# Optimization experiments

Measured on AMD Instinct MI355X. Metric: run time of the kernel, lower is better.

The kernel has to match this reference:

```python
import jax, jax.numpy as jnp
import numpy as np

NTOKENS = 50257
NHID = 1024
NPC = int(np.ceil(np.sqrt(NTOKENS)))            # 225 tokens per class
NCLASSES = int(np.ceil(NTOKENS / NPC))          # 224 classes
BATCH = 1024
INITRANGE = 0.1


def setup_inputs() -> dict:
    key = jax.random.key(0)
    k1, k2, k3, k4 = jax.random.split(key, 4)
    inputs = jax.random.normal(k1, (BATCH, NHID), dtype=jnp.float32)
    labels = jax.random.randint(k2, (BATCH,), 0, NTOKENS, dtype=jnp.int64)
    layer_top_W = jax.random.uniform(k3, (NHID, NCLASSES), minval=-INITRANGE, maxval=INITRANGE, dtype=jnp.float32)
    layer_top_b = jnp.zeros((NCLASSES,), dtype=jnp.float32)
    layer_bottom_W = jax.random.uniform(k4, (NCLASSES, NHID, NPC), minval=-INITRANGE, maxval=INITRANGE, dtype=jnp.float32)
    layer_bottom_b = jnp.zeros((NCLASSES, NPC), dtype=jnp.float32)
    return {
        "inputs": inputs,
        "labels": labels,
        "layer_top_W": layer_top_W,
        "layer_top_b": layer_top_b,
        "layer_bottom_W": layer_bottom_W,
        "layer_bottom_b": layer_bottom_b,
    }


def reference(inputs, labels, layer_top_W, layer_top_b, layer_bottom_W, layer_bottom_b):
    batch_size = inputs.shape[0]
    # decompose label into (class, within-class) position; old-torch `/` on Long == floor div
    pos_top = labels // NPC            # [B]
    pos_bottom = labels % NPC          # [B]

    # top-level class distribution: [B, nclasses]
    top_logits = inputs @ layer_top_W + layer_top_b
    top_probs = jax.nn.softmax(top_logits, axis=1)

    # gather per-sample class weight slices and do batched matvec:
    # layer_bottom_W[pos_top]: [B, nhid, npc]
    bottom_logits = jnp.einsum("bd,bdc->bc", inputs, layer_bottom_W[pos_top]) + layer_bottom_b[pos_top]
    bottom_probs = jax.nn.softmax(bottom_logits, axis=1)

    rows = jnp.arange(batch_size)
    target_probs = top_probs[rows, pos_top] * bottom_probs[rows, pos_bottom]  # [B]
    return target_probs
```

## Files before the change

kernel.cpp:

```cpp
#include <hip/hip_runtime.h>
#include <math.h>

#define NTOK 50257
#define NHID 1024
#define NPC  225
#define NCLS 224
#define BATCH 1024

#define WS_ORDER_OFS 16
#define WS_ITEMS_OFS 8192
#define WS_PTOP_OFS  16384
#define MAX_ITEMS    352

__global__ __launch_bounds__(256) void k0_group(const int* __restrict__ labels,
                                                int* __restrict__ ws)
{
    __shared__ int cnt[256];
    __shared__ int scan[256];
    __shared__ int iscan[256];
    __shared__ int cur[256];
    const int tid = threadIdx.x;

    cnt[tid] = 0;
    __syncthreads();
    for (int i = tid; i < BATCH; i += 256)
        atomicAdd(&cnt[labels[i] / NPC], 1);
    __syncthreads();

    const int myc = (tid < NCLS) ? cnt[tid] : 0;
    const int myi = (myc + 7) >> 3;
    scan[tid]  = myc;
    iscan[tid] = myi;
    __syncthreads();
    for (int off = 1; off < 256; off <<= 1) {
        int a = (tid >= off) ? scan[tid - off]  : 0;
        int b = (tid >= off) ? iscan[tid - off] : 0;
        __syncthreads();
        scan[tid]  += a;
        iscan[tid] += b;
        __syncthreads();
    }
    const int sbase = scan[tid]  - myc;
    const int ibase = iscan[tid] - myi;
    if (tid == 255) ws[0] = iscan[255];
    cur[tid] = sbase;

    int4* items = (int4*)((char*)ws + WS_ITEMS_OFS);
    if (tid < NCLS) {
        for (int t = 0; t < myi; ++t)
            items[ibase + t] = make_int4(tid, sbase + 8 * t, min(8, myc - 8 * t), 0);
    }
    __syncthreads();

    int* order = ws + WS_ORDER_OFS;
    for (int i = tid; i < BATCH; i += 256) {
        int c = labels[i] / NPC;
        int p = atomicAdd(&cur[c], 1);
        order[p] = i;
    }
}

__global__ __launch_bounds__(256) void k1_top(const float* __restrict__ X,
                                              const int* __restrict__ labels,
                                              const float* __restrict__ Wt,
                                              const float* __restrict__ bt,
                                              float* __restrict__ ptop)
{
    __shared__ __align__(16) float smem[12288];
    const int tid  = threadIdx.x;
    const int wave = tid >> 6;
    const int lane = tid & 63;
    const int sbase = blockIdx.x * 8;

    for (int idx = tid; idx < 8 * NHID; idx += 256) {
        int j = idx >> 10, dd = idx & 1023;
        smem[dd * 12 + j] = X[(sbase + j) * NHID + dd];
    }
    __syncthreads();

    float acc[8][4];
#pragma unroll
    for (int j = 0; j < 8; ++j)
#pragma unroll
        for (int k = 0; k < 4; ++k) acc[j][k] = 0.f;

    const int d0 = wave * 256;
#pragma unroll 4
    for (int dd = d0; dd < d0 + 256; ++dd) {
        float w[4];
        w[0] = Wt[dd * NCLS + lane];
        w[1] = Wt[dd * NCLS + lane + 64];
        w[2] = Wt[dd * NCLS + lane + 128];
        w[3] = (lane < 32) ? Wt[dd * NCLS + lane + 192] : 0.f;
        float4 a = *(const float4*)&smem[dd * 12 + 0];
        float4 b = *(const float4*)&smem[dd * 12 + 4];
        float xi[8] = {a.x, a.y, a.z, a.w, b.x, b.y, b.z, b.w};
#pragma unroll
        for (int j = 0; j < 8; ++j)
#pragma unroll
            for (int k = 0; k < 4; ++k) acc[j][k] += xi[j] * w[k];
    }
    __syncthreads();

    float* red = smem;
#pragma unroll
    for (int j = 0; j < 8; ++j)
#pragma unroll
        for (int k = 0; k < 4; ++k) {
            int c = lane + 64 * k;
            if (c < NCLS) red[(wave * 8 + j) * 232 + c] = acc[j][k];
        }
    __syncthreads();

    for (int jj = 0; jj < 2; ++jj) {
        const int j = wave * 2 + jj;
        const int s = sbase + j;
        float v[4];
#pragma unroll
        for (int k = 0; k < 4; ++k) {
            int c = lane + 64 * k;
            v[k] = (c < NCLS)
                     ? (red[(0 * 8 + j) * 232 + c] + red[(1 * 8 + j) * 232 + c] +
                        red[(2 * 8 + j) * 232 + c] + red[(3 * 8 + j) * 232 + c] + bt[c])
                     : -INFINITY;
        }
        float m = fmaxf(fmaxf(v[0], v[1]), fmaxf(v[2], v[3]));
        for (int o = 32; o > 0; o >>= 1) m = fmaxf(m, __shfl_xor(m, o));
        float e = expf(v[0] - m) + expf(v[1] - m) + expf(v[2] - m) + expf(v[3] - m);
        for (int o = 32; o > 0; o >>= 1) e += __shfl_xor(e, o);
        const int pt = labels[s] / NPC;
        if (lane == (pt & 63))
            ptop[s] = expf(v[pt >> 6] - m) / e;
    }
}

__global__ __launch_bounds__(256) void k2_bottom(const float* __restrict__ X,
                                                 const int* __restrict__ labels,
                                                 const float* __restrict__ Wb,
                                                 const float* __restrict__ bb,
                                                 const int* __restrict__ ws,
                                                 const float* __restrict__ ptop,
                                                 float* __restrict__ out)
{
    __shared__ __align__(16) float smem[12288];
    const int nitems = ws[0];
    if ((int)blockIdx.x >= nitems) return;
    const int4 item = ((const int4*)((const char*)ws + WS_ITEMS_OFS))[blockIdx.x];
    const int cls = item.x, s0 = item.y, nt = item.z;
    const int* order = ws + WS_ORDER_OFS;

    const int tid  = threadIdx.x;
    const int wave = tid >> 6;
    const int lane = tid & 63;

    for (int idx = tid; idx < 8 * NHID; idx += 256) {
        int j = idx >> 10, dd = idx & 1023;
        float v = 0.f;
        if (j < nt) v = X[order[s0 + j] * NHID + dd];
        smem[dd * 12 + j] = v;
    }
    __syncthreads();

    float acc[8][4];
#pragma unroll
    for (int j = 0; j < 8; ++j)
#pragma unroll
        for (int k = 0; k < 4; ++k) acc[j][k] = 0.f;

    const float* W = Wb + (size_t)cls * (NHID * NPC);
    const int d0 = wave * 256;
#pragma unroll 4
    for (int dd = d0; dd < d0 + 256; ++dd) {
        float w[4];
        w[0] = W[dd * NPC + lane];
        w[1] = W[dd * NPC + lane + 64];
        w[2] = W[dd * NPC + lane + 128];
        w[3] = (lane + 192 < NPC) ? W[dd * NPC + lane + 192] : 0.f;
        float4 a = *(const float4*)&smem[dd * 12 + 0];
        float4 b = *(const float4*)&smem[dd * 12 + 4];
        float xi[8] = {a.x, a.y, a.z, a.w, b.x, b.y, b.z, b.w};
#pragma unroll
        for (int j = 0; j < 8; ++j)
#pragma unroll
            for (int k = 0; k < 4; ++k) acc[j][k] += xi[j] * w[k];
    }
    __syncthreads();

    float* red = smem;
#pragma unroll
    for (int j = 0; j < 8; ++j)
#pragma unroll
        for (int k = 0; k < 4; ++k) {
            int c = lane + 64 * k;
            if (c < NPC) red[(wave * 8 + j) * 232 + c] = acc[j][k];
        }
    __syncthreads();

    for (int jj = 0; jj < 2; ++jj) {
        const int j = wave * 2 + jj;
        if (j >= nt) continue;
        const int s = order[s0 + j];
        float v[4];
#pragma unroll
        for (int k = 0; k < 4; ++k) {
            int c = lane + 64 * k;
            v[k] = (c < NPC)
                     ? (red[(0 * 8 + j) * 232 + c] + red[(1 * 8 + j) * 232 + c] +
                        red[(2 * 8 + j) * 232 + c] + red[(3 * 8 + j) * 232 + c] +
                        bb[cls * NPC + c])
                     : -INFINITY;
        }
        float m = fmaxf(fmaxf(v[0], v[1]), fmaxf(v[2], v[3]));
        for (int o = 32; o > 0; o >>= 1) m = fmaxf(m, __shfl_xor(m, o));
        float e = expf(v[0] - m) + expf(v[1] - m) + expf(v[2] - m) + expf(v[3] - m);
        for (int o = 32; o > 0; o >>= 1) e += __shfl_xor(e, o);
        const int pb = labels[s] % NPC;
        if (lane == (pb & 63))
            out[s] = ptop[s] * (expf(v[pb >> 6] - m) / e);
    }
}

extern "C" void kernel_launch(void* const* d_in, const int* in_sizes, int n_in,
                              void* d_out, int out_size, void* d_ws, size_t ws_size,
                              hipStream_t stream)
{
    const float* X      = (const float*)d_in[0];
    const int*   labels = (const int*)  d_in[1];
    const float* Wt     = (const float*)d_in[2];
    const float* bt     = (const float*)d_in[3];
    const float* Wb     = (const float*)d_in[4];
    const float* bb     = (const float*)d_in[5];
    float* out = (float*)d_out;
    int*   ws  = (int*)d_ws;
    float* ptop = (float*)((char*)d_ws + WS_PTOP_OFS);

    hipLaunchKernelGGL(k0_group, dim3(1), dim3(256), 0, stream, labels, ws);
    hipLaunchKernelGGL(k1_top, dim3(BATCH / 8), dim3(256), 0, stream,
                       X, labels, Wt, bt, ptop);
    hipLaunchKernelGGL(k2_bottom, dim3(MAX_ITEMS), dim3(256), 0, stream,
                       X, labels, Wb, bb, ws, ptop, out);
}
```

Baseline: 362.7 us.

## Double block size to 512 threads, prefetch weights, vectorize X staging

Both matvec kernels now use 8 waves per block instead of 4, each wave covering 128 hidden dims, and combine the two halves with a two-stage shared-memory reduction. Weight rows are register-prefetched one iteration ahead so loads overlap the FMAs. X rows are staged with float4 loads, and the shared logic moves into a templated device function. The aim is more memory-level parallelism on the weight stream, at the cost of an extra barrier and higher register use under the 512-thread launch bound.

```diff
diff --git a/kernel.cpp b/kernel.cpp
--- a/kernel.cpp
+++ b/kernel.cpp
@@ -60,81 +60,130 @@
     }
 }
 
-__global__ __launch_bounds__(256) void k1_top(const float* __restrict__ X,
-                                              const int* __restrict__ labels,
-                                              const float* __restrict__ Wt,
-                                              const float* __restrict__ bt,
-                                              float* __restrict__ ptop)
-{
-    __shared__ __align__(16) float smem[12288];
-    const int tid  = threadIdx.x;
-    const int wave = tid >> 6;
-    const int lane = tid & 63;
-    const int sbase = blockIdx.x * 8;
-
-    for (int idx = tid; idx < 8 * NHID; idx += 256) {
-        int j = idx >> 10, dd = idx & 1023;
-        smem[dd * 12 + j] = X[(sbase + j) * NHID + dd];
-    }
-    __syncthreads();
-
+template <int LD, int COLS>
+__device__ __forceinline__ void block_matvec8_softmax(
+    float* __restrict__ sm,
+    const float* __restrict__ W,
+    const float* __restrict__ bias,
+    int wave, int lane,
+    int nt,
+    const int* __restrict__ s_ids,
+    const int* __restrict__ labels,
+    bool bottom,
+    const float* __restrict__ ptop,
+    float* __restrict__ outp)
+{
     float acc[8][4];
 #pragma unroll
     for (int j = 0; j < 8; ++j)
 #pragma unroll
         for (int k = 0; k < 4; ++k) acc[j][k] = 0.f;
 
-    const int d0 = wave * 256;
+    const int c0 = lane, c1 = lane + 64, c2 = lane + 128, c3 = lane + 192;
+    const bool m3 = (c3 < COLS);
+    const int d0 = wave * 128;
+    const float* Wr = W + (size_t)d0 * LD;
+
+    float w0 = Wr[c0], w1 = Wr[c1], w2 = Wr[c2], w3 = m3 ? Wr[c3] : 0.f;
 #pragma unroll 4
-    for (int dd = d0; dd < d0 + 256; ++dd) {
-        float w[4];
-        w[0] = Wt[dd * NCLS + lane];
-        w[1] = Wt[dd * NCLS + lane + 64];
-        w[2] = Wt[dd * NCLS + lane + 128];
-        w[3] = (lane < 32) ? Wt[dd * NCLS + lane + 192] : 0.f;
-        float4 a = *(const float4*)&smem[dd * 12 + 0];
-        float4 b = *(const float4*)&smem[dd * 12 + 4];
-        float xi[8] = {a.x, a.y, a.z, a.w, b.x, b.y, b.z, b.w};
+    for (int dd = 0; dd < 128; ++dd) {
+        const float cw0 = w0, cw1 = w1, cw2 = w2, cw3 = w3;
+        const float* nr = Wr + (size_t)min(dd + 1, 127) * LD;
+        w0 = nr[c0]; w1 = nr[c1]; w2 = nr[c2]; w3 = m3 ? nr[c3] : 0.f;
+        const float4 a = *(const float4*)&sm[(d0 + dd) * 12 + 0];
+        const float4 b = *(const float4*)&sm[(d0 + dd) * 12 + 4];
+        const float xi[8] = {a.x, a.y, a.z, a.w, b.x, b.y, b.z, b.w};
+#pragma unroll
+        for (int j = 0; j < 8; ++j) {
+            acc[j][0] = fmaf(xi[j], cw0, acc[j][0]);
+            acc[j][1] = fmaf(xi[j], cw1, acc[j][1]);
+            acc[j][2] = fmaf(xi[j], cw2, acc[j][2]);
+            acc[j][3] = fmaf(xi[j], cw3, acc[j][3]);
+        }
+    }
+    __syncthreads();
+
+    float* red = sm;
+    if (wave >= 4) {
 #pragma unroll
         for (int j = 0; j < 8; ++j)
 #pragma unroll
-            for (int k = 0; k < 4; ++k) acc[j][k] += xi[j] * w[k];
-    }
-    __syncthreads();
-
-    float* red = smem;
-#pragma unroll
-    for (int j = 0; j < 8; ++j)
+            for (int k = 0; k < 4; ++k) {
+                int c = lane + 64 * k;
+                if (c < COLS) red[((wave - 4) * 8 + j) * 232 + c] = acc[j][k];
+            }
+    }
+    __syncthreads();
+    if (wave < 4) {
+#pragma unroll
+        for (int j = 0; j < 8; ++j)
+#pragma unroll
+            for (int k = 0; k < 4; ++k) {
+                int c = lane + 64 * k;
+                if (c < COLS)
+                    red[(wave * 8 + j) * 232 + c] += acc[j][k];
+            }
+    }
+    __syncthreads();
+
+    const int j = wave;
+    if (j < nt) {
+        const int s = s_ids[j];
+        float v[4];
 #pragma unroll
         for (int k = 0; k < 4; ++k) {
             int c = lane + 64 * k;
-            if (c < NCLS) red[(wave * 8 + j) * 232 + c] = acc[j][k];
-        }
-    __syncthreads();
-
-    for (int jj = 0; jj < 2; ++jj) {
-        const int j = wave * 2 + jj;
-        const int s = sbase + j;
-        float v[4];
-#pragma unroll
-        for (int k = 0; k < 4; ++k) {
-            int c = lane + 64 * k;
-            v[k] = (c < NCLS)
+            v[k] = (c < COLS)
                      ? (red[(0 * 8 + j) * 232 + c] + red[(1 * 8 + j) * 232 + c] +
-                        red[(2 * 8 + j) * 232 + c] + red[(3 * 8 + j) * 232 + c] + bt[c])
+                        red[(2 * 8 + j) * 232 + c] + red[(3 * 8 + j) * 232 + c] +
+                        bias[c])
                      : -INFINITY;
         }
         float m = fmaxf(fmaxf(v[0], v[1]), fmaxf(v[2], v[3]));
         for (int o = 32; o > 0; o >>= 1) m = fmaxf(m, __shfl_xor(m, o));
         float e = expf(v[0] - m) + expf(v[1] - m) + expf(v[2] - m) + expf(v[3] - m);
         for (int o = 32; o > 0; o >>= 1) e += __shfl_xor(e, o);
-        const int pt = labels[s] / NPC;
-        if (lane == (pt & 63))
-            ptop[s] = expf(v[pt >> 6] - m) / e;
-    }
-}
-
-__global__ __launch_bounds__(256) void k2_bottom(const float* __restrict__ X,
+        const int lab = labels[s];
+        const int tgt = bottom ? (lab % NPC) : (lab / NPC);
+        if (lane == (tgt & 63)) {
+            float p = expf(v[tgt >> 6] - m) / e;
+            outp[s] = bottom ? (ptop[s] * p) : p;
+        }
+    }
+}
+
+__global__ __launch_bounds__(512) void k1_top(const float* __restrict__ X,
+                                              const int* __restrict__ labels,
+                                              const float* __restrict__ Wt,
+                                              const float* __restrict__ bt,
+                                              float* __restrict__ ptop)
+{
+    __shared__ __align__(16) float smem[12288];
+    const int tid  = threadIdx.x;
+    const int wave = tid >> 6;
+    const int lane = tid & 63;
+    const int sbase = blockIdx.x * 8;
+
+    for (int idx = tid; idx < 2048; idx += 512) {
+        const int j  = idx >> 8;
+        const int d4 = idx & 255;
+        const float4 v = ((const float4*)&X[(size_t)(sbase + j) * NHID])[d4];
+        smem[(4 * d4 + 0) * 12 + j] = v.x;
+        smem[(4 * d4 + 1) * 12 + j] = v.y;
+        smem[(4 * d4 + 2) * 12 + j] = v.z;
+        smem[(4 * d4 + 3) * 12 + j] = v.w;
+    }
+    __syncthreads();
+
+    int s_ids[8];
+#pragma unroll
+    for (int j = 0; j < 8; ++j) s_ids[j] = sbase + j;
+
+    block_matvec8_softmax<NCLS, NCLS>(smem, Wt, bt, wave, lane, 8, s_ids,
+                                      labels, false, nullptr, ptop);
+}
+
+__global__ __launch_bounds__(512) void k2_bottom(const float* __restrict__ X,
                                                  const int* __restrict__ labels,
                                                  const float* __restrict__ Wb,
                                                  const float* __restrict__ bb,
@@ -153,71 +202,25 @@
     const int wave = tid >> 6;
     const int lane = tid & 63;
 
-    for (int idx = tid; idx < 8 * NHID; idx += 256) {
-        int j = idx >> 10, dd = idx & 1023;
-        float v = 0.f;
-        if (j < nt) v = X[order[s0 + j] * NHID + dd];
-        smem[dd * 12 + j] = v;
-    }
-    __syncthreads();
-
-    float acc[8][4];
-#pragma unroll
-    for (int j = 0; j < 8; ++j)
-#pragma unroll
-        for (int k = 0; k < 4; ++k) acc[j][k] = 0.f;
+    int s_ids[8];
+#pragma unroll
+    for (int j = 0; j < 8; ++j) s_ids[j] = (j < nt) ? order[s0 + j] : 0;
+
+    for (int idx = tid; idx < 2048; idx += 512) {
+        const int j  = idx >> 8;
+        const int d4 = idx & 255;
+        float4 v = make_float4(0.f, 0.f, 0.f, 0.f);
+        if (j < nt) v = ((const float4*)&X[(size_t)s_ids[j] * NHID])[d4];
+        smem[(4 * d4 + 0) * 12 + j] = v.x;
+        smem[(4 * d4 + 1) * 12 + j] = v.y;
+        smem[(4 * d4 + 2) * 12 + j] = v.z;
+        smem[(4 * d4 + 3) * 12 + j] = v.w;
+    }
+    __syncthreads();
 
     const float* W = Wb + (size_t)cls * (NHID * NPC);
-    const int d0 = wave * 256;
-#pragma unroll 4
-    for (int dd = d0; dd < d0 + 256; ++dd) {
-        float w[4];
-        w[0] = W[dd * NPC + lane];
-        w[1] = W[dd * NPC + lane + 64];
-        w[2] = W[dd * NPC + lane + 128];
-        w[3] = (lane + 192 < NPC) ? W[dd * NPC + lane + 192] : 0.f;
-        float4 a = *(const float4*)&smem[dd * 12 + 0];
-        float4 b = *(const float4*)&smem[dd * 12 + 4];
-        float xi[8] = {a.x, a.y, a.z, a.w, b.x, b.y, b.z, b.w};
-#pragma unroll
-        for (int j = 0; j < 8; ++j)
-#pragma unroll
-            for (int k = 0; k < 4; ++k) acc[j][k] += xi[j] * w[k];
-    }
-    __syncthreads();
-
-    float* red = smem;
-#pragma unroll
-    for (int j = 0; j < 8; ++j)
-#pragma unroll
-        for (int k = 0; k < 4; ++k) {
-            int c = lane + 64 * k;
-            if (c < NPC) red[(wave * 8 + j) * 232 + c] = acc[j][k];
-        }
-    __syncthreads();
-
-    for (int jj = 0; jj < 2; ++jj) {
-        const int j = wave * 2 + jj;
-        if (j >= nt) continue;
-        const int s = order[s0 + j];
-        float v[4];
-#pragma unroll
-        for (int k = 0; k < 4; ++k) {
-            int c = lane + 64 * k;
-            v[k] = (c < NPC)
-                     ? (red[(0 * 8 + j) * 232 + c] + red[(1 * 8 + j) * 232 + c] +
-                        red[(2 * 8 + j) * 232 + c] + red[(3 * 8 + j) * 232 + c] +
-                        bb[cls * NPC + c])
-                     : -INFINITY;
-        }
-        float m = fmaxf(fmaxf(v[0], v[1]), fmaxf(v[2], v[3]));
-        for (int o = 32; o > 0; o >>= 1) m = fmaxf(m, __shfl_xor(m, o));
-        float e = expf(v[0] - m) + expf(v[1] - m) + expf(v[2] - m) + expf(v[3] - m);
-        for (int o = 32; o > 0; o >>= 1) e += __shfl_xor(e, o);
-        const int pb = labels[s] % NPC;
-        if (lane == (pb & 63))
-            out[s] = ptop[s] * (expf(v[pb >> 6] - m) / e);
-    }
+    block_matvec8_softmax<NPC, NPC>(smem, W, bb + cls * NPC, wave, lane, nt,
+                                    s_ids, labels, true, ptop, out);
 }
 
 extern "C" void kernel_launch(void* const* d_in, const int* in_sizes, int n_in,
@@ -235,8 +238,8 @@
     float* ptop = (float*)((char*)d_ws + WS_PTOP_OFS);
 
     hipLaunchKernelGGL(k0_group, dim3(1), dim3(256), 0, stream, labels, ws);
-    hipLaunchKernelGGL(k1_top, dim3(BATCH / 8), dim3(256), 0, stream,
+    hipLaunchKernelGGL(k1_top, dim3(BATCH / 8), dim3(512), 0, stream,
                        X, labels, Wt, bt, ptop);
-    hipLaunchKernelGGL(k2_bottom, dim3(MAX_ITEMS), dim3(256), 0, stream,
+    hipLaunchKernelGGL(k2_bottom, dim3(MAX_ITEMS), dim3(512), 0, stream,
                        X, labels, Wb, bb, ws, ptop, out);
 }
```

New measurement: 330.4 us. -8.9%, faster.
